# Kernel optimization log

Measured on AMD Instinct MI355X. Metric: run time of the kernel, lower is better.

The kernel has to match this reference:

```python
import jax, jax.numpy as jnp
import numpy as np

H = 1024
B = 8
T = 2048

def setup_inputs() -> dict:
    key = jax.random.key(0)
    ks = jax.random.split(key, 12)
    s = 1.0 / np.sqrt(H)
    return {
        "x": jax.random.normal(ks[0], (B, T, H), dtype=jnp.float32),
        "time_decay": jax.random.normal(ks[1], (H,), dtype=jnp.float32) * 0.1,
        "time_first": jax.random.normal(ks[2], (H,), dtype=jnp.float32) * 0.1,
        "time_mix_key": jax.random.uniform(ks[3], (1, 1, H), dtype=jnp.float32),
        "time_mix_value": jax.random.uniform(ks[4], (1, 1, H), dtype=jnp.float32),
        "time_mix_receptance": jax.random.uniform(ks[5], (1, 1, H), dtype=jnp.float32),
        "Wk": jax.random.normal(ks[6], (H, H), dtype=jnp.float32) * s,
        "Wv": jax.random.normal(ks[7], (H, H), dtype=jnp.float32) * s,
        "Wr": jax.random.normal(ks[8], (H, H), dtype=jnp.float32) * s,
        "Wo": jax.random.normal(ks[9], (H, H), dtype=jnp.float32) * s,
        "bo": jax.random.normal(ks[10], (H,), dtype=jnp.float32) * 0.01,
    }

def reference(x, time_decay, time_first, time_mix_key, time_mix_value,
              time_mix_receptance, Wk, Wv, Wr, Wo, bo):
    # time shift: shifted[:, t] = x[:, t-1], shifted[:, 0] = 0
    shifted = jnp.pad(x, ((0, 0), (1, 0), (0, 0)))[:, :-1]
    k_in = x * time_mix_key + shifted * (1.0 - time_mix_key)
    v_in = x * time_mix_value + shifted * (1.0 - time_mix_value)
    r_in = x * time_mix_receptance + shifted * (1.0 - time_mix_receptance)
    k = jnp.einsum('bth,oh->bto', k_in, Wk)
    v = jnp.einsum('bth,oh->bto', v_in, Wv)
    r = jax.nn.sigmoid(jnp.einsum('bth,oh->bto', r_in, Wr))

    td = jnp.exp(-jnp.exp(time_decay))  # (H,)

    def step(carry, kv):
        num, den = carry            # (B, H) each
        k_t, v_t = kv               # (B, H) each
        e = jnp.exp(time_first + k_t)
        out_t = (num + e * v_t) / (den + e)
        ek = jnp.exp(k_t)
        return (td * num + ek * v_t, td * den + ek), out_t

    init = (jnp.zeros((x.shape[0], x.shape[2]), x.dtype),
            jnp.zeros((x.shape[0], x.shape[2]), x.dtype))
    # scan over time: (T, B, H)
    _, wkv = jax.lax.scan(step, init, (k.transpose(1, 0, 2), v.transpose(1, 0, 2)))
    wkv = wkv.transpose(1, 0, 2)    # (B, T, H)

    return jnp.einsum('bth,oh->bto', r * wkv, Wo) + bo
```

## Files before the change

### kernel.cpp

```cpp
#include <hip/hip_runtime.h>
#include <hip/hip_bf16.h>
#include <cstdint>
#include <cstddef>

#define HH 1024
#define BB 8
#define TT 2048
#define MM (BB*TT)
#define CC 64
#define LL (TT/CC)

typedef __attribute__((ext_vector_type(8))) short bf16x8;
typedef __attribute__((ext_vector_type(16))) float f32x16;

__device__ __forceinline__ unsigned short f2bf(float f) {
  union { float f; unsigned u; } v; v.f = f;
  return (unsigned short)((v.u + 0x7fffu + ((v.u >> 16) & 1u)) >> 16);
}
__device__ __forceinline__ float bf2f(unsigned short s) {
  union { float f; unsigned u; } v; v.u = ((unsigned)s) << 16;
  return v.f;
}

__device__ __forceinline__ void load_lds16(const void* g, void* l) {
  __builtin_amdgcn_global_load_lds((const __attribute__((address_space(1))) void*)g,
                                   (__attribute__((address_space(3))) void*)l,
                                   16, 0, 0);
}

__global__ __launch_bounds__(256) void conv_w(const float* __restrict__ Wk,
    const float* __restrict__ Wv, const float* __restrict__ Wr,
    const float* __restrict__ Wo, unsigned short* __restrict__ dst) {
  const int i = (blockIdx.x * 256 + threadIdx.x) * 4;
  const float* src = blockIdx.y == 0 ? Wk : blockIdx.y == 1 ? Wv : blockIdx.y == 2 ? Wr : Wo;
  const float4 v = *(const float4*)(src + i);
  ushort4 o; o.x = f2bf(v.x); o.y = f2bf(v.y); o.z = f2bf(v.z); o.w = f2bf(v.w);
  *(ushort4*)(dst + (size_t)blockIdx.y * HH * HH + i) = o;
}

__global__ __launch_bounds__(256) void mix_kernel(const float* __restrict__ x,
    const float* __restrict__ tmk, const float* __restrict__ tmv, const float* __restrict__ tmr,
    unsigned short* __restrict__ kin, unsigned short* __restrict__ vin,
    unsigned short* __restrict__ rin) {
  const int gid = blockIdx.x * 256 + threadIdx.x;
  const size_t e0 = (size_t)gid * 4;
  const int h = (int)(e0 & (HH - 1));
  const int t = (int)((e0 >> 10) & (TT - 1));
  const float4 xv = *(const float4*)(x + e0);
  float4 sv = make_float4(0.f, 0.f, 0.f, 0.f);
  if (t != 0) sv = *(const float4*)(x + e0 - HH);
  const float4 k4 = *(const float4*)(tmk + h);
  const float4 v4 = *(const float4*)(tmv + h);
  const float4 r4 = *(const float4*)(tmr + h);
  ushort4 ko, vo, ro;
  ko.x = f2bf(sv.x + k4.x * (xv.x - sv.x)); ko.y = f2bf(sv.y + k4.y * (xv.y - sv.y));
  ko.z = f2bf(sv.z + k4.z * (xv.z - sv.z)); ko.w = f2bf(sv.w + k4.w * (xv.w - sv.w));
  vo.x = f2bf(sv.x + v4.x * (xv.x - sv.x)); vo.y = f2bf(sv.y + v4.y * (xv.y - sv.y));
  vo.z = f2bf(sv.z + v4.z * (xv.z - sv.z)); vo.w = f2bf(sv.w + v4.w * (xv.w - sv.w));
  ro.x = f2bf(sv.x + r4.x * (xv.x - sv.x)); ro.y = f2bf(sv.y + r4.y * (xv.y - sv.y));
  ro.z = f2bf(sv.z + r4.z * (xv.z - sv.z)); ro.w = f2bf(sv.w + r4.w * (xv.w - sv.w));
  *(ushort4*)(kin + e0) = ko;
  *(ushort4*)(vin + e0) = vo;
  *(ushort4*)(rin + e0) = ro;
}

__device__ __forceinline__ void gemm_core32(const unsigned short* __restrict__ Ag,
                                            const unsigned short* __restrict__ Bg,
                                            int m0, int n0,
                                            unsigned short* As, unsigned short* Bs,
                                            f32x16 acc[2][2]) {
  const int tid = threadIdx.x;
  const int lane = tid & 63;
  const int w = tid >> 6;
  const int K = HH;
  const int c0 = tid, c1 = 256 + tid;
  const int r0 = c0 >> 2, s0 = c0 & 3, q0 = s0 ^ ((r0 >> 1) & 3);
  const int r1 = c1 >> 2, s1 = c1 & 3, q1 = s1 ^ ((r1 >> 1) & 3);
  const unsigned short* ga0 = Ag + (size_t)(m0 + r0) * K + q0 * 8;
  const unsigned short* ga1 = Ag + (size_t)(m0 + r1) * K + q1 * 8;
  const unsigned short* gb0 = Bg + (size_t)(n0 + r0) * K + q0 * 8;
  const unsigned short* gb1 = Bg + (size_t)(n0 + r1) * K + q1 * 8;
  unsigned short* la0 = As + (size_t)w * 512;
  unsigned short* la1 = As + 2048 + (size_t)w * 512;
  unsigned short* lb0 = Bs + (size_t)w * 512;
  unsigned short* lb1 = Bs + 2048 + (size_t)w * 512;
  const int wm = w >> 1, wn = w & 1;
  const int l31 = lane & 31, lh = lane >> 5;
  const int arow0 = wm * 64 + l31;
  const int brow0 = wn * 64 + l31;

  for (int kt = 0; kt < K; kt += 32) {
    load_lds16(ga0 + kt, la0);
    load_lds16(ga1 + kt, la1);
    load_lds16(gb0 + kt, lb0);
    load_lds16(gb1 + kt, lb1);
    __syncthreads();
    bf16x8 af[2][2], bfr[2][2];
#pragma unroll
    for (int c = 0; c < 2; c++) {
      const int kq = c * 2 + lh;
#pragma unroll
      for (int mi = 0; mi < 2; mi++) {
        const int ar = arow0 + mi * 32;
        af[mi][c] = *(const bf16x8*)(As + ar * 32 + (kq ^ ((ar >> 1) & 3)) * 8);
      }
#pragma unroll
      for (int nj = 0; nj < 2; nj++) {
        const int br = brow0 + nj * 32;
        bfr[nj][c] = *(const bf16x8*)(Bs + br * 32 + (kq ^ ((br >> 1) & 3)) * 8);
      }
    }
#pragma unroll
    for (int c = 0; c < 2; c++)
#pragma unroll
      for (int mi = 0; mi < 2; mi++)
#pragma unroll
        for (int nj = 0; nj < 2; nj++)
          acc[mi][nj] = __builtin_amdgcn_mfma_f32_32x32x16_bf16(af[mi][c], bfr[nj][c],
                                                                acc[mi][nj], 0, 0, 0);
    __syncthreads();
  }
}

__device__ __forceinline__ void swizzle_mn(int x, int& m0, int& n0) {
  const int xcd = x & 7;
  const int t = x >> 3;
  const int bn = t & 7;
  const int bml = t >> 3;
  m0 = (xcd * 16 + bml) * 128;
  n0 = bn * 128;
}

__global__ __launch_bounds__(256) void gemm_kvr(const unsigned short* __restrict__ kin,
    const unsigned short* __restrict__ vin, const unsigned short* __restrict__ rin,
    const unsigned short* __restrict__ Wbf,
    unsigned short* __restrict__ kb, unsigned short* __restrict__ vb,
    unsigned short* __restrict__ rb) {
  __shared__ unsigned short As[128 * 32];
  __shared__ unsigned short Bs[128 * 32];
  const int z = blockIdx.y;
  const unsigned short* Ag = z == 0 ? kin : (z == 1 ? vin : rin);
  const unsigned short* Bg = Wbf + (size_t)z * HH * HH;
  unsigned short* Cg = z == 0 ? kb : (z == 1 ? vb : rb);
  int m0, n0; swizzle_mn(blockIdx.x, m0, n0);
  f32x16 acc[2][2] = {};
  gemm_core32(Ag, Bg, m0, n0, As, Bs, acc);
  const int lane = threadIdx.x & 63, w = threadIdx.x >> 6;
  const int wm = w >> 1, wn = w & 1, l31 = lane & 31, lh = lane >> 5;
  const bool sig = (z == 2);
#pragma unroll
  for (int mi = 0; mi < 2; mi++)
#pragma unroll
    for (int nj = 0; nj < 2; nj++) {
      const int col = n0 + wn * 64 + nj * 32 + l31;
      const int rb0 = m0 + wm * 64 + mi * 32 + 4 * lh;
#pragma unroll
      for (int reg = 0; reg < 16; reg++) {
        const int row = rb0 + (reg & 3) + 8 * (reg >> 2);
        float vv = acc[mi][nj][reg];
        if (sig) vv = 1.0f / (1.0f + __expf(-vv));
        Cg[(size_t)row * HH + col] = f2bf(vv);
      }
    }
}

__global__ __launch_bounds__(256) void gemm_o(const unsigned short* __restrict__ Ag,
    const unsigned short* __restrict__ Bg, const float* __restrict__ bias,
    float* __restrict__ C) {
  __shared__ unsigned short As[128 * 32];
  __shared__ unsigned short Bs[128 * 32];
  int m0, n0; swizzle_mn(blockIdx.x, m0, n0);
  f32x16 acc[2][2] = {};
  gemm_core32(Ag, Bg, m0, n0, As, Bs, acc);
  const int lane = threadIdx.x & 63, w = threadIdx.x >> 6;
  const int wm = w >> 1, wn = w & 1, l31 = lane & 31, lh = lane >> 5;
#pragma unroll
  for (int mi = 0; mi < 2; mi++)
#pragma unroll
    for (int nj = 0; nj < 2; nj++) {
      const int col = n0 + wn * 64 + nj * 32 + l31;
      const float bv = bias[col];
      const int rb0 = m0 + wm * 64 + mi * 32 + 4 * lh;
#pragma unroll
      for (int reg = 0; reg < 16; reg++) {
        const int row = rb0 + (reg & 3) + 8 * (reg >> 2);
        C[(size_t)row * HH + col] = acc[mi][nj][reg] + bv;
      }
    }
}

__global__ __launch_bounds__(256) void wkv_part(const unsigned short* __restrict__ k,
    const unsigned short* __restrict__ v, const float* __restrict__ tdec,
    float* __restrict__ pnum, float* __restrict__ pden) {
  const int gid = blockIdx.x * 256 + threadIdx.x;
  const int h = gid & (HH - 1);
  const int bh = gid & (BB * HH - 1);
  const int b = (gid >> 10) & (BB - 1);
  const int c = gid >> 13;
  const float td = __expf(-__expf(tdec[h]));
  size_t idx = (size_t)b * TT * HH + (size_t)(c * LL) * HH + h;
  float num = 0.f, den = 0.f;
#pragma unroll 8
  for (int i = 0; i < LL; ++i, idx += HH) {
    const float ek = __expf(bf2f(k[idx]));
    const float vt = bf2f(v[idx]);
    num = td * num + ek * vt;
    den = td * den + ek;
  }
  pnum[(size_t)c * (BB * HH) + bh] = num;
  pden[(size_t)c * (BB * HH) + bh] = den;
}

__global__ __launch_bounds__(256) void wkv_scan(const float* __restrict__ tdec,
    float* __restrict__ pnum, float* __restrict__ pden) {
  const int bh = blockIdx.x * 256 + threadIdx.x;
  const int h = bh & (HH - 1);
  const float ed = __expf(tdec[h]);
  const float tdL = __expf(-ed * (float)LL);
  float num = 0.f, den = 0.f;
#pragma unroll 8
  for (int c = 0; c < CC; ++c) {
    const size_t o = (size_t)c * (BB * HH) + bh;
    const float tn = pnum[o], td_ = pden[o];
    pnum[o] = num; pden[o] = den;
    num = tdL * num + tn;
    den = tdL * den + td_;
  }
}

__global__ __launch_bounds__(256) void wkv_final(const unsigned short* __restrict__ k,
    const unsigned short* __restrict__ v, const unsigned short* __restrict__ r,
    const float* __restrict__ tdec, const float* __restrict__ tfst,
    const float* __restrict__ pnum, const float* __restrict__ pden,
    unsigned short* __restrict__ rwkv) {
  const int gid = blockIdx.x * 256 + threadIdx.x;
  const int h = gid & (HH - 1);
  const int bh = gid & (BB * HH - 1);
  const int b = (gid >> 10) & (BB - 1);
  const int c = gid >> 13;
  const float td = __expf(-__expf(tdec[h]));
  const float etf = __expf(tfst[h]);
  float num = pnum[(size_t)c * (BB * HH) + bh];
  float den = pden[(size_t)c * (BB * HH) + bh];
  size_t idx = (size_t)b * TT * HH + (size_t)(c * LL) * HH + h;
#pragma unroll 4
  for (int i = 0; i < LL; ++i, idx += HH) {
    const float ek = __expf(bf2f(k[idx]));
    const float vt = bf2f(v[idx]);
    const float rt = bf2f(r[idx]);
    const float e = ek * etf;
    const float inv = __builtin_amdgcn_rcpf(den + e);
    const float outv = (num + e * vt) * inv;
    num = td * num + ek * vt;
    den = td * den + ek;
    rwkv[idx] = f2bf(outv * rt);
  }
}

extern "C" void kernel_launch(void* const* d_in, const int* in_sizes, int n_in,
                              void* d_out, int out_size, void* d_ws, size_t ws_size,
                              hipStream_t stream) {
  (void)in_sizes; (void)n_in; (void)out_size; (void)ws_size;
  const float* x    = (const float*)d_in[0];
  const float* tdec = (const float*)d_in[1];
  const float* tfst = (const float*)d_in[2];
  const float* tmk  = (const float*)d_in[3];
  const float* tmv  = (const float*)d_in[4];
  const float* tmr  = (const float*)d_in[5];
  const float* Wk   = (const float*)d_in[6];
  const float* Wv   = (const float*)d_in[7];
  const float* Wr   = (const float*)d_in[8];
  const float* Wo   = (const float*)d_in[9];
  const float* bo   = (const float*)d_in[10];
  float* out = (float*)d_out;

  char* ws = (char*)d_ws;
  const size_t MiB = (size_t)1 << 20;
  unsigned short* Wbf = (unsigned short*)(ws);
  unsigned short* kin = (unsigned short*)(ws + 8 * MiB);
  unsigned short* vin = (unsigned short*)(ws + 40 * MiB);
  unsigned short* rin = (unsigned short*)(ws + 72 * MiB);
  unsigned short* rb  = (unsigned short*)(ws + 104 * MiB);
  unsigned short* kb = (unsigned short*)out;
  unsigned short* vb = kb + (size_t)MM * HH;
  unsigned short* rwkv = kin;
  float* pnum = (float*)(ws + 40 * MiB);
  float* pden = (float*)(ws + 42 * MiB);

  hipLaunchKernelGGL(conv_w, dim3(1024, 4), dim3(256), 0, stream, Wk, Wv, Wr, Wo, Wbf);
  hipLaunchKernelGGL(mix_kernel, dim3(16384), dim3(256), 0, stream,
                     x, tmk, tmv, tmr, kin, vin, rin);
  hipLaunchKernelGGL(gemm_kvr, dim3(1024, 3), dim3(256), 0, stream,
                     kin, vin, rin, Wbf, kb, vb, rb);
  hipLaunchKernelGGL(wkv_part, dim3(2048), dim3(256), 0, stream,
                     kb, vb, tdec, pnum, pden);
  hipLaunchKernelGGL(wkv_scan, dim3(32), dim3(256), 0, stream,
                     tdec, pnum, pden);
  hipLaunchKernelGGL(wkv_final, dim3(2048), dim3(256), 0, stream,
                     kb, vb, rb, tdec, tfst, pnum, pden, rwkv);
  hipLaunchKernelGGL(gemm_o, dim3(1024), dim3(256), 0, stream,
                     rwkv, Wbf + (size_t)3 * HH * HH, bo, out);
}
```

Before: 384.5 us.

## Replace 128x128 GEMM core with 256x256 double-buffered pipelined MFMA tiles

Rewrites the shared GEMM core used by the k/v/r projections and the output projection. It moves from 128x128 tiles with K-step 32 and 4 waves to 256x256 tiles with K-step 64 and 8 waves, using 16x16x32 bf16 MFMAs. Global-to-LDS loads are double-buffered and interleaved with compute quadrants, with explicit vmcnt/lgkmcnt waits, barriers and s_setprio. The aim is more data reuse per LDS byte and hiding load latency behind MFMA work. In exchange it uses 128 KB of LDS per block and more registers, and the grid drops to 256 blocks per GEMM, which is about one block per CU.

New measurement: 363.1 us. 5.6% less time.

```diff
diff --git a/kernel.cpp b/kernel.cpp
--- a/kernel.cpp
+++ b/kernel.cpp
@@ -11,7 +11,7 @@
 #define LL (TT/CC)
 
 typedef __attribute__((ext_vector_type(8))) short bf16x8;
-typedef __attribute__((ext_vector_type(16))) float f32x16;
+typedef __attribute__((ext_vector_type(4))) float f32x4;
 
 __device__ __forceinline__ unsigned short f2bf(float f) {
   union { float f; unsigned u; } v; v.f = f;
@@ -64,128 +64,182 @@
   *(ushort4*)(rin + e0) = ro;
 }
 
-__device__ __forceinline__ void gemm_core32(const unsigned short* __restrict__ Ag,
-                                            const unsigned short* __restrict__ Bg,
-                                            int m0, int n0,
-                                            unsigned short* As, unsigned short* Bs,
-                                            f32x16 acc[2][2]) {
+
+#define BAR()   do { asm volatile("" ::: "memory"); __builtin_amdgcn_s_barrier(); \
+                     asm volatile("" ::: "memory"); } while (0)
+#define LGKM0() asm volatile("s_waitcnt lgkmcnt(0)" ::: "memory")
+#define VM6()   asm volatile("s_waitcnt vmcnt(6)" ::: "memory")
+#define VM0()   asm volatile("s_waitcnt vmcnt(0)" ::: "memory")
+
+__device__ __forceinline__ void stA(const unsigned short* __restrict__ Ag, int m0, int kt,
+                                    unsigned short* buf, int h, int w, int rl, int scol) {
+#pragma unroll
+  for (int l = 0; l < 2; ++l) {
+    const int row = l * 128 + h * 64 + w * 8;
+    load_lds16(Ag + (size_t)(m0 + row + rl) * HH + kt + scol, buf + row * 64);
+  }
+}
+__device__ __forceinline__ void stB(const unsigned short* __restrict__ Bg, int n0, int kt,
+                                    unsigned short* buf, int h, int w, int rl, int scol) {
+#pragma unroll
+  for (int l = 0; l < 2; ++l) {
+    const int row = (2 * (l * 2 + (w >> 2)) + h) * 32 + (w & 3) * 8;
+    load_lds16(Bg + (size_t)(n0 + row + rl) * HH + kt + scol, buf + row * 64);
+  }
+}
+
+template<int MH>
+__device__ __forceinline__ void rdA(const unsigned short* buf, bf16x8 (&af)[4][2],
+                                    int wm, int l15, int kq, int swz) {
+#pragma unroll
+  for (int fm = 0; fm < 4; ++fm)
+#pragma unroll
+    for (int kk = 0; kk < 2; ++kk)
+      af[fm][kk] = *(const bf16x8*)(buf + (wm * 128 + MH * 64 + fm * 16 + l15) * 64
+                                        + ((kk * 32 + kq * 8) ^ swz));
+}
+template<int NH>
+__device__ __forceinline__ void rdB(const unsigned short* buf, bf16x8 (&bfr)[2][2][2],
+                                    int wn, int l15, int kq, int swz) {
+#pragma unroll
+  for (int fn = 0; fn < 2; ++fn)
+#pragma unroll
+    for (int kk = 0; kk < 2; ++kk)
+      bfr[NH][fn][kk] = *(const bf16x8*)(buf + (wn * 64 + NH * 32 + fn * 16 + l15) * 64
+                                             + ((kk * 32 + kq * 8) ^ swz));
+}
+template<int MH, int NH>
+__device__ __forceinline__ void mfmaQ(f32x4 (&acc)[8][4], const bf16x8 (&af)[4][2],
+                                      const bf16x8 (&bfr)[2][2][2]) {
+  __builtin_amdgcn_s_setprio(1);
+#pragma unroll
+  for (int kk = 0; kk < 2; ++kk)
+#pragma unroll
+    for (int fm = 0; fm < 4; ++fm)
+#pragma unroll
+      for (int fn = 0; fn < 2; ++fn)
+        acc[MH * 4 + fm][NH * 2 + fn] = __builtin_amdgcn_mfma_f32_16x16x32_bf16(
+            af[fm][kk], bfr[NH][fn][kk], acc[MH * 4 + fm][NH * 2 + fn], 0, 0, 0);
+  __builtin_amdgcn_s_setprio(0);
+}
+
+__device__ __forceinline__ void gemm256(const unsigned short* __restrict__ Ag,
+                                        const unsigned short* __restrict__ Bg,
+                                        const int m0, const int n0,
+                                        unsigned short* As, unsigned short* Bs,
+                                        f32x4 (&acc)[8][4]) {
   const int tid = threadIdx.x;
   const int lane = tid & 63;
   const int w = tid >> 6;
-  const int K = HH;
-  const int c0 = tid, c1 = 256 + tid;
-  const int r0 = c0 >> 2, s0 = c0 & 3, q0 = s0 ^ ((r0 >> 1) & 3);
-  const int r1 = c1 >> 2, s1 = c1 & 3, q1 = s1 ^ ((r1 >> 1) & 3);
-  const unsigned short* ga0 = Ag + (size_t)(m0 + r0) * K + q0 * 8;
-  const unsigned short* ga1 = Ag + (size_t)(m0 + r1) * K + q1 * 8;
-  const unsigned short* gb0 = Bg + (size_t)(n0 + r0) * K + q0 * 8;
-  const unsigned short* gb1 = Bg + (size_t)(n0 + r1) * K + q1 * 8;
-  unsigned short* la0 = As + (size_t)w * 512;
-  unsigned short* la1 = As + 2048 + (size_t)w * 512;
-  unsigned short* lb0 = Bs + (size_t)w * 512;
-  unsigned short* lb1 = Bs + 2048 + (size_t)w * 512;
-  const int wm = w >> 1, wn = w & 1;
-  const int l31 = lane & 31, lh = lane >> 5;
-  const int arow0 = wm * 64 + l31;
-  const int brow0 = wn * 64 + l31;
-
-  for (int kt = 0; kt < K; kt += 32) {
-    load_lds16(ga0 + kt, la0);
-    load_lds16(ga1 + kt, la1);
-    load_lds16(gb0 + kt, lb0);
-    load_lds16(gb1 + kt, lb1);
-    __syncthreads();
-    bf16x8 af[2][2], bfr[2][2];
-#pragma unroll
-    for (int c = 0; c < 2; c++) {
-      const int kq = c * 2 + lh;
-#pragma unroll
-      for (int mi = 0; mi < 2; mi++) {
-        const int ar = arow0 + mi * 32;
-        af[mi][c] = *(const bf16x8*)(As + ar * 32 + (kq ^ ((ar >> 1) & 3)) * 8);
-      }
-#pragma unroll
-      for (int nj = 0; nj < 2; nj++) {
-        const int br = brow0 + nj * 32;
-        bfr[nj][c] = *(const bf16x8*)(Bs + br * 32 + (kq ^ ((br >> 1) & 3)) * 8);
-      }
-    }
-#pragma unroll
-    for (int c = 0; c < 2; c++)
-#pragma unroll
-      for (int mi = 0; mi < 2; mi++)
-#pragma unroll
-        for (int nj = 0; nj < 2; nj++)
-          acc[mi][nj] = __builtin_amdgcn_mfma_f32_32x32x16_bf16(af[mi][c], bfr[nj][c],
-                                                                acc[mi][nj], 0, 0, 0);
-    __syncthreads();
-  }
-}
-
-__device__ __forceinline__ void swizzle_mn(int x, int& m0, int& n0) {
-  const int xcd = x & 7;
-  const int t = x >> 3;
-  const int bn = t & 7;
-  const int bml = t >> 3;
-  m0 = (xcd * 16 + bml) * 128;
-  n0 = bn * 128;
-}
-
-__global__ __launch_bounds__(256) void gemm_kvr(const unsigned short* __restrict__ kin,
+  const int wm = w >> 2, wn = w & 3;
+  const int l15 = lane & 15, kq = lane >> 4;
+  const int swz = ((lane >> 2) & 1) << 4;
+  const int rl = lane >> 3;
+  const int scol = ((lane & 7) * 8) ^ (((lane >> 5) & 1) << 4);
+  unsigned short* const A0 = As;
+  unsigned short* const A1 = As + 256 * 64;
+  unsigned short* const B0 = Bs;
+  unsigned short* const B1 = Bs + 256 * 64;
+  bf16x8 af[4][2], bfr[2][2][2];
+
+  stA(Ag, m0, 0, A0, 0, w, rl, scol);
+  stB(Bg, n0, 0, B0, 0, w, rl, scol);
+  stB(Bg, n0, 0, B0, 1, w, rl, scol);
+  stA(Ag, m0, 0, A0, 1, w, rl, scol);
+  stA(Ag, m0, 64, A1, 0, w, rl, scol);
+  stB(Bg, n0, 64, B1, 0, w, rl, scol);
+  stB(Bg, n0, 64, B1, 1, w, rl, scol);
+  VM6(); BAR();
+
+#pragma unroll 1
+  for (int i = 0; i < 8; ++i) {
+    const int tb1 = ((2 * i + 1) * 64) & (HH - 1);
+    const int tn0 = ((2 * i + 2) * 64) & (HH - 1);
+    const int tn1 = ((2 * i + 3) * 64) & (HH - 1);
+    rdA<0>(A0, af, wm, l15, kq, swz); rdB<0>(B0, bfr, wn, l15, kq, swz);
+    stA(Ag, m0, tb1, A1, 1, w, rl, scol);
+    BAR(); LGKM0(); mfmaQ<0, 0>(acc, af, bfr); BAR();
+    rdB<1>(B0, bfr, wn, l15, kq, swz);
+    stA(Ag, m0, tn0, A0, 0, w, rl, scol);
+    BAR(); LGKM0(); mfmaQ<0, 1>(acc, af, bfr); BAR();
+    rdA<1>(A0, af, wm, l15, kq, swz);
+    stB(Bg, n0, tn0, B0, 0, w, rl, scol);
+    BAR(); LGKM0(); mfmaQ<1, 1>(acc, af, bfr); BAR();
+    stB(Bg, n0, tn0, B0, 1, w, rl, scol);
+    VM6(); BAR(); LGKM0(); mfmaQ<1, 0>(acc, af, bfr); BAR();
+    rdA<0>(A1, af, wm, l15, kq, swz); rdB<0>(B1, bfr, wn, l15, kq, swz);
+    stA(Ag, m0, tn0, A0, 1, w, rl, scol);
+    BAR(); LGKM0(); mfmaQ<0, 0>(acc, af, bfr); BAR();
+    rdB<1>(B1, bfr, wn, l15, kq, swz);
+    stA(Ag, m0, tn1, A1, 0, w, rl, scol);
+    BAR(); LGKM0(); mfmaQ<0, 1>(acc, af, bfr); BAR();
+    rdA<1>(A1, af, wm, l15, kq, swz);
+    stB(Bg, n0, tn1, B1, 0, w, rl, scol);
+    BAR(); LGKM0(); mfmaQ<1, 1>(acc, af, bfr); BAR();
+    stB(Bg, n0, tn1, B1, 1, w, rl, scol);
+    VM6(); BAR(); LGKM0(); mfmaQ<1, 0>(acc, af, bfr); BAR();
+  }
+  VM0();
+}
+
+__device__ __forceinline__ void swizzle_mn256(int x, int& m0, int& n0) {
+  const int wg = (x & 7) * 32 + (x >> 3);
+  m0 = (wg >> 2) * 256;
+  n0 = (wg & 3) * 256;
+}
+
+__global__ __launch_bounds__(512, 2) void gemm_kvr(const unsigned short* __restrict__ kin,
     const unsigned short* __restrict__ vin, const unsigned short* __restrict__ rin,
     const unsigned short* __restrict__ Wbf,
     unsigned short* __restrict__ kb, unsigned short* __restrict__ vb,
     unsigned short* __restrict__ rb) {
-  __shared__ unsigned short As[128 * 32];
-  __shared__ unsigned short Bs[128 * 32];
+  __shared__ unsigned short As[2 * 256 * 64];
+  __shared__ unsigned short Bs[2 * 256 * 64];
   const int z = blockIdx.y;
   const unsigned short* Ag = z == 0 ? kin : (z == 1 ? vin : rin);
   const unsigned short* Bg = Wbf + (size_t)z * HH * HH;
   unsigned short* Cg = z == 0 ? kb : (z == 1 ? vb : rb);
-  int m0, n0; swizzle_mn(blockIdx.x, m0, n0);
-  f32x16 acc[2][2] = {};
-  gemm_core32(Ag, Bg, m0, n0, As, Bs, acc);
+  int m0, n0; swizzle_mn256(blockIdx.x, m0, n0);
+  f32x4 acc[8][4] = {};
+  gemm256(Ag, Bg, m0, n0, As, Bs, acc);
   const int lane = threadIdx.x & 63, w = threadIdx.x >> 6;
-  const int wm = w >> 1, wn = w & 1, l31 = lane & 31, lh = lane >> 5;
+  const int wm = w >> 2, wn = w & 3, l15 = lane & 15, lq = lane >> 4;
   const bool sig = (z == 2);
 #pragma unroll
-  for (int mi = 0; mi < 2; mi++)
-#pragma unroll
-    for (int nj = 0; nj < 2; nj++) {
-      const int col = n0 + wn * 64 + nj * 32 + l31;
-      const int rb0 = m0 + wm * 64 + mi * 32 + 4 * lh;
-#pragma unroll
-      for (int reg = 0; reg < 16; reg++) {
-        const int row = rb0 + (reg & 3) + 8 * (reg >> 2);
-        float vv = acc[mi][nj][reg];
+  for (int fm = 0; fm < 8; ++fm)
+#pragma unroll
+    for (int fn = 0; fn < 4; ++fn) {
+      const int col = n0 + wn * 64 + fn * 16 + l15;
+      const int r0 = m0 + wm * 128 + fm * 16 + lq * 4;
+#pragma unroll
+      for (int j = 0; j < 4; ++j) {
+        float vv = acc[fm][fn][j];
         if (sig) vv = 1.0f / (1.0f + __expf(-vv));
-        Cg[(size_t)row * HH + col] = f2bf(vv);
+        Cg[(size_t)(r0 + j) * HH + col] = f2bf(vv);
       }
     }
 }
 
-__global__ __launch_bounds__(256) void gemm_o(const unsigned short* __restrict__ Ag,
+__global__ __launch_bounds__(512, 2) void gemm_o(const unsigned short* __restrict__ Ag,
     const unsigned short* __restrict__ Bg, const float* __restrict__ bias,
     float* __restrict__ C) {
-  __shared__ unsigned short As[128 * 32];
-  __shared__ unsigned short Bs[128 * 32];
-  int m0, n0; swizzle_mn(blockIdx.x, m0, n0);
-  f32x16 acc[2][2] = {};
-  gemm_core32(Ag, Bg, m0, n0, As, Bs, acc);
+  __shared__ unsigned short As[2 * 256 * 64];
+  __shared__ unsigned short Bs[2 * 256 * 64];
+  int m0, n0; swizzle_mn256(blockIdx.x, m0, n0);
+  f32x4 acc[8][4] = {};
+  gemm256(Ag, Bg, m0, n0, As, Bs, acc);
   const int lane = threadIdx.x & 63, w = threadIdx.x >> 6;
-  const int wm = w >> 1, wn = w & 1, l31 = lane & 31, lh = lane >> 5;
-#pragma unroll
-  for (int mi = 0; mi < 2; mi++)
-#pragma unroll
-    for (int nj = 0; nj < 2; nj++) {
-      const int col = n0 + wn * 64 + nj * 32 + l31;
+  const int wm = w >> 2, wn = w & 3, l15 = lane & 15, lq = lane >> 4;
+#pragma unroll
+  for (int fm = 0; fm < 8; ++fm)
+#pragma unroll
+    for (int fn = 0; fn < 4; ++fn) {
+      const int col = n0 + wn * 64 + fn * 16 + l15;
       const float bv = bias[col];
-      const int rb0 = m0 + wm * 64 + mi * 32 + 4 * lh;
-#pragma unroll
-      for (int reg = 0; reg < 16; reg++) {
-        const int row = rb0 + (reg & 3) + 8 * (reg >> 2);
-        C[(size_t)row * HH + col] = acc[mi][nj][reg] + bv;
-      }
+      const int r0 = m0 + wm * 128 + fm * 16 + lq * 4;
+#pragma unroll
+      for (int j = 0; j < 4; ++j)
+        C[(size_t)(r0 + j) * HH + col] = acc[fm][fn][j] + bv;
     }
 }
 
@@ -290,7 +344,7 @@
   hipLaunchKernelGGL(conv_w, dim3(1024, 4), dim3(256), 0, stream, Wk, Wv, Wr, Wo, Wbf);
   hipLaunchKernelGGL(mix_kernel, dim3(16384), dim3(256), 0, stream,
                      x, tmk, tmv, tmr, kin, vin, rin);
-  hipLaunchKernelGGL(gemm_kvr, dim3(1024, 3), dim3(256), 0, stream,
+  hipLaunchKernelGGL(gemm_kvr, dim3(256, 3), dim3(512), 0, stream,
                      kin, vin, rin, Wbf, kb, vb, rb);
   hipLaunchKernelGGL(wkv_part, dim3(2048), dim3(256), 0, stream,
                      kb, vb, tdec, pnum, pden);
@@ -298,6 +352,6 @@
                      tdec, pnum, pden);
   hipLaunchKernelGGL(wkv_final, dim3(2048), dim3(256), 0, stream,
                      kb, vb, rb, tdec, tfst, pnum, pden, rwkv);
-  hipLaunchKernelGGL(gemm_o, dim3(1024), dim3(256), 0, stream,
+  hipLaunchKernelGGL(gemm_o, dim3(256), dim3(512), 0, stream,
                      rwkv, Wbf + (size_t)3 * HH * HH, bo, out);
 }
```
